# Kernel optimization log

Measured on AMD Instinct MI355X. Metric: run time of the kernel, lower is better.

## Reference

```python
import jax, jax.numpy as jnp
import numpy as np

N, E, G = 100000, 1600000, 1024
BN_EPS = 1e-5
NEG_SLOPE = 0.2


def setup_inputs() -> dict:
    key = jax.random.key(0)
    ks = jax.random.split(key, 8)
    x = jax.random.normal(ks[0], (N, 128), dtype=jnp.float32)
    edge_index = jax.random.randint(ks[1], (2, E), 0, N, dtype=jnp.int64)
    batch = jnp.sort(jax.random.randint(ks[2], (N,), 0, G, dtype=jnp.int64))
    Wl = jax.random.normal(ks[3], (3, 128, 128), dtype=jnp.float32) * 0.08
    bl = jnp.zeros((3, 128), dtype=jnp.float32)
    Wr = jax.random.normal(ks[4], (3, 128, 128), dtype=jnp.float32) * 0.08
    bn_gamma = jnp.ones((3, 128), dtype=jnp.float32)
    bn_beta = jnp.zeros((3, 128), dtype=jnp.float32)
    bn2_gamma = jnp.ones((128,), dtype=jnp.float32)
    bn2_beta = jnp.zeros((128,), dtype=jnp.float32)
    fc_W = jax.random.normal(ks[5], (128, 64), dtype=jnp.float32) * 0.08
    fc_b = jnp.zeros((64,), dtype=jnp.float32)
    return {"x": x, "edge_index": edge_index, "batch": batch, "Wl": Wl, "bl": bl,
            "Wr": Wr, "bn_gamma": bn_gamma, "bn_beta": bn_beta,
            "bn2_gamma": bn2_gamma, "bn2_beta": bn2_beta, "fc_W": fc_W, "fc_b": fc_b}


def _batch_norm(h, gamma, beta):
    # training-mode BatchNorm1d: batch statistics, biased variance
    mu = jnp.mean(h, axis=0)
    var = jnp.mean((h - mu) ** 2, axis=0)
    return gamma * (h - mu) * jax.lax.rsqrt(var + BN_EPS) + beta


def reference(x, edge_index, batch, Wl, bl, Wr, bn_gamma, bn_beta,
              bn2_gamma, bn2_beta, fc_W, fc_b):
    src, dst = edge_index[0], edge_index[1]
    # in-degree of each destination node (for mean aggregation)
    deg = jax.ops.segment_sum(jnp.ones((E,), dtype=x.dtype), dst, num_segments=N)
    inv_deg = jnp.where(deg > 0, 1.0 / jnp.maximum(deg, 1.0), 0.0)[:, None]  # [N,1]
    h = x
    for i in range(3):
        # SAGEConv: out = lin_l(mean_{j in N(i)} h_j) + lin_r(h_i)
        agg = jax.ops.segment_sum(h[src], dst, num_segments=N) * inv_deg  # [N,H]
        h = agg @ Wl[i] + bl[i] + h @ Wr[i]
        h = jax.nn.leaky_relu(_batch_norm(h, bn_gamma[i], bn_beta[i]), NEG_SLOPE)
        # dropout omitted (eval-mode / deterministic reference)
    pooled = jax.ops.segment_sum(h, batch, num_segments=G)  # [G,H] global_add_pool
    out = _batch_norm(pooled, bn2_gamma, bn2_beta) @ fc_W + fc_b  # [G,latent]
    return out
```

## Files before the change

kernel.cpp:

```cpp
#include <hip/hip_runtime.h>

#define HD 128
#define NCOPY 32
#define BSH 8
#define BSZ 256
#define EPB 4096

typedef __attribute__((ext_vector_type(8))) short short8;
typedef __attribute__((ext_vector_type(4))) float f32x4;

union ABu { unsigned long long u[2]; short8 s8; };

__device__ inline float bf2f(ushort u) {
    union { unsigned int i; float f; } x; x.i = ((unsigned int)u) << 16; return x.f;
}
__device__ inline float bflo(unsigned int u) {
    union { unsigned int i; float f; } x; x.i = u << 16; return x.f;
}
__device__ inline float bfhi(unsigned int u) {
    union { unsigned int i; float f; } x; x.i = u & 0xffff0000u; return x.f;
}
__device__ inline ushort f2bf(float f) {
    union { float f; unsigned int i; } x; x.f = f;
    unsigned int r = x.i + 0x7FFF + ((x.i >> 16) & 1);
    return (ushort)(r >> 16);
}


__global__ __launch_bounds__(256) void kp_count(const int* __restrict__ dst,
                                                int* __restrict__ bucketCount, int E, int NB) {
    __shared__ int hist[512];
    for (int i = threadIdx.x; i < NB; i += 256) hist[i] = 0;
    __syncthreads();
    int e0 = blockIdx.x * EPB;
#pragma unroll
    for (int j = 0; j < 16; ++j) {
        int e = e0 + j * 256 + threadIdx.x;
        if (e < E) atomicAdd(&hist[dst[e] >> BSH], 1);
    }
    __syncthreads();
    for (int i = threadIdx.x; i < NB; i += 256)
        if (hist[i]) atomicAdd(&bucketCount[i], hist[i]);
}

__global__ void kp_scan(const int* __restrict__ bucketCount, int* __restrict__ bucketBase,
                        int* __restrict__ gCursor, int NB, int E) {
    __shared__ int lds[512];
    int tid = threadIdx.x;
    int v = (tid < NB) ? bucketCount[tid] : 0;
    lds[tid] = v;
    __syncthreads();
    for (int off = 1; off < 512; off <<= 1) {
        int t = 0;
        if (tid >= off) t = lds[tid - off];
        __syncthreads();
        if (tid >= off) lds[tid] += t;
        __syncthreads();
    }
    int excl = lds[tid] - v;
    if (tid < NB) { bucketBase[tid] = excl; gCursor[tid] = excl; }
    if (tid == 0) bucketBase[NB] = E;
}

__global__ __launch_bounds__(256) void kp_part(const int* __restrict__ src,
                                               const int* __restrict__ dst,
                                               int* __restrict__ gCursor,
                                               unsigned int* __restrict__ packed, int E, int NB) {
    __shared__ int hist[512], lbase[512], lcur[512];
    for (int i = threadIdx.x; i < NB; i += 256) hist[i] = 0;
    __syncthreads();
    int e0 = blockIdx.x * EPB;
    int b[16]; unsigned int w[16];
#pragma unroll
    for (int j = 0; j < 16; ++j) {
        int e = e0 + j * 256 + threadIdx.x;
        b[j] = -1;
        if (e < E) {
            int d = dst[e];
            int s = src[e];
            b[j] = d >> BSH;
            w[j] = (unsigned int)s | (((unsigned int)d & (BSZ - 1)) << 17);
            atomicAdd(&hist[b[j]], 1);
        }
    }
    __syncthreads();
    for (int i = threadIdx.x; i < NB; i += 256) {
        int c = hist[i];
        lbase[i] = c ? atomicAdd(&gCursor[i], c) : 0;
        lcur[i] = 0;
    }
    __syncthreads();
#pragma unroll
    for (int j = 0; j < 16; ++j) {
        if (b[j] >= 0) {
            int r = atomicAdd(&lcur[b[j]], 1);
            packed[lbase[b[j]] + r] = w[j];
        }
    }
}

__global__ __launch_bounds__(256) void kp_degscan(const unsigned int* __restrict__ packed,
                                                  const int* __restrict__ bucketBase,
                                                  int* __restrict__ rowptr,
                                                  float* __restrict__ inv, int N, int E) {
    __shared__ int dcnt[BSZ];
    __shared__ int scn[BSZ];
    int bkt = blockIdx.x;
    int tid = threadIdx.x;
    int n0 = bkt << BSH;
    dcnt[tid] = 0;
    __syncthreads();
    int beg = bucketBase[bkt], end = bucketBase[bkt + 1];
    for (int e = beg + tid; e < end; e += 256)
        atomicAdd(&dcnt[packed[e] >> 17], 1);
    __syncthreads();
    int v = dcnt[tid];
    scn[tid] = v;
    __syncthreads();
    for (int off = 1; off < 256; off <<= 1) {
        int t = 0;
        if (tid >= off) t = scn[tid - off];
        __syncthreads();
        if (tid >= off) scn[tid] += t;
        __syncthreads();
    }
    int n = n0 + tid;
    if (n < N) {
        rowptr[n] = beg + scn[tid] - v;
        inv[n] = (v > 0) ? (1.0f / (float)v) : 0.0f;
    }
    if (bkt == 0 && tid == 0) rowptr[N] = E;
}

__global__ __launch_bounds__(256) void kp_fill(const unsigned int* __restrict__ packed,
                                               const int* __restrict__ bucketBase,
                                               const int* __restrict__ rowptr,
                                               int* __restrict__ csr, int N) {
    __shared__ int rp[BSZ];
    __shared__ int cur[BSZ];
    int bkt = blockIdx.x;
    int n0 = bkt << BSH;
    for (int i = threadIdx.x; i < BSZ; i += 256) {
        int n = n0 + i;
        rp[i] = (n < N) ? rowptr[n] : 0;
        cur[i] = 0;
    }
    __syncthreads();
    int beg = bucketBase[bkt], end = bucketBase[bkt + 1];
    for (int e = beg + threadIdx.x; e < end; e += 256) {
        unsigned int wv = packed[e];
        int ld = wv >> 17;
        int s = (int)(wv & 0x1FFFF);
        int p = atomicAdd(&cur[ld], 1);
        csr[rp[ld] + p] = s;
    }
}

__global__ void k_cvt(const float* __restrict__ in, ushort* __restrict__ out, int total4) {
    int i = blockIdx.x * blockDim.x + threadIdx.x;
    int stride = gridDim.x * blockDim.x;
    for (int idx = i; idx < total4; idx += stride) {
        float4 v = ((const float4*)in)[idx];
        ushort4 o;
        o.x = f2bf(v.x); o.y = f2bf(v.y); o.z = f2bf(v.z); o.w = f2bf(v.w);
        ((ushort4*)out)[idx] = o;
    }
}

__global__ void k_wt(const float* __restrict__ Wl, const float* __restrict__ Wr,
                     ushort* __restrict__ WT, int total) {
    int i = blockIdx.x * blockDim.x + threadIdx.x;
    if (i >= total) return;
    int l = i >> 15;
    int rem = i & 32767;
    int col = rem >> 8;
    int k = rem & 255;
    float v = (k < 128) ? Wl[l * 16384 + k * 128 + col] : Wr[l * 16384 + (k - 128) * 128 + col];
    WT[i] = f2bf(v);
}

__global__ __launch_bounds__(256) void k_agg(const ushort* __restrict__ h,
                                             const int* __restrict__ rowptr,
                                             const int* __restrict__ csr,
                                             const float* __restrict__ inv,
                                             ushort* __restrict__ agg, int N) {
    int node = blockIdx.x * 4 + (threadIdx.x >> 6);
    if (node >= N) return;
    int lane = threadIdx.x & 63;
    int g = lane >> 4, ln = lane & 15;
    int beg = rowptr[node], end = rowptr[node + 1];
    float a[8], b[8], c[8], d[8];
#pragma unroll
    for (int j = 0; j < 8; ++j) { a[j] = 0.f; b[j] = 0.f; c[j] = 0.f; d[j] = 0.f; }
    for (int e = beg + g; e < end; e += 16) {
        int s0 = csr[e];
        uint4 v0 = *(const uint4*)&h[(size_t)s0 * HD + ln * 8];
        int e1 = e + 4, e2 = e + 8, e3 = e + 12;
        if (e1 < end) {
            int s1 = csr[e1];
            uint4 v1 = *(const uint4*)&h[(size_t)s1 * HD + ln * 8];
            b[0] += bflo(v1.x); b[1] += bfhi(v1.x);
            b[2] += bflo(v1.y); b[3] += bfhi(v1.y);
            b[4] += bflo(v1.z); b[5] += bfhi(v1.z);
            b[6] += bflo(v1.w); b[7] += bfhi(v1.w);
        }
        if (e2 < end) {
            int s2 = csr[e2];
            uint4 v2 = *(const uint4*)&h[(size_t)s2 * HD + ln * 8];
            c[0] += bflo(v2.x); c[1] += bfhi(v2.x);
            c[2] += bflo(v2.y); c[3] += bfhi(v2.y);
            c[4] += bflo(v2.z); c[5] += bfhi(v2.z);
            c[6] += bflo(v2.w); c[7] += bfhi(v2.w);
        }
        if (e3 < end) {
            int s3 = csr[e3];
            uint4 v3 = *(const uint4*)&h[(size_t)s3 * HD + ln * 8];
            d[0] += bflo(v3.x); d[1] += bfhi(v3.x);
            d[2] += bflo(v3.y); d[3] += bfhi(v3.y);
            d[4] += bflo(v3.z); d[5] += bfhi(v3.z);
            d[6] += bflo(v3.w); d[7] += bfhi(v3.w);
        }
        a[0] += bflo(v0.x); a[1] += bfhi(v0.x);
        a[2] += bflo(v0.y); a[3] += bfhi(v0.y);
        a[4] += bflo(v0.z); a[5] += bfhi(v0.z);
        a[6] += bflo(v0.w); a[7] += bfhi(v0.w);
    }
#pragma unroll
    for (int j = 0; j < 8; ++j) {
        a[j] += b[j] + (c[j] + d[j]);
        a[j] += __shfl_xor(a[j], 16);
        a[j] += __shfl_xor(a[j], 32);
    }
    if (lane < 16) {
        float iv = inv[node];
        ushort o[8];
#pragma unroll
        for (int j = 0; j < 8; ++j) o[j] = f2bf(a[j] * iv);
        *(uint4*)&agg[(size_t)node * HD + ln * 8] = *(uint4*)o;
    }
}

__global__ __launch_bounds__(256) void k_gemm(
        const ushort* __restrict__ X1, const ushort* __restrict__ X2,
        const ushort* __restrict__ WT, const float* __restrict__ bias,
        ushort* __restrict__ out, float* __restrict__ stats, int N) {
    __shared__ ushort As[128 * 40];
    __shared__ ushort Bs[128 * 40];
    int tid = threadIdx.x;
    int lane = tid & 63, wid = tid >> 6;
    int wr = wid >> 1, wc = wid & 1;
    int ln15 = lane & 15, kg = lane >> 4;
    int rbase = blockIdx.x * 128;

    f32x4 acc[4][4];
#pragma unroll
    for (int m = 0; m < 4; ++m)
#pragma unroll
        for (int nn = 0; nn < 4; ++nn) acc[m][nn] = (f32x4){0.f, 0.f, 0.f, 0.f};

    for (int c = 0; c < 8; ++c) {
        const ushort* X = (c < 4) ? X1 : X2;
        int cb = (c & 3) * 32;
#pragma unroll
        for (int p = 0; p < 2; ++p) {
            int g = tid + p * 256;
            int r = g >> 2, q = g & 3;
            int grow = rbase + r;
            uint4 v = {0u, 0u, 0u, 0u};
            if (grow < N) v = *(const uint4*)&X[(size_t)grow * HD + cb + q * 8];
            *(uint4*)&As[r * 40 + q * 8] = v;
        }
#pragma unroll
        for (int p = 0; p < 2; ++p) {
            int g = tid + p * 256;
            int col = g >> 2, q = g & 3;
            *(uint4*)&Bs[col * 40 + q * 8] = *(const uint4*)&WT[col * 256 + c * 32 + q * 8];
        }
        __syncthreads();
        short8 af[4], bfr[4];
#pragma unroll
        for (int m = 0; m < 4; ++m) {
            int row = wr * 64 + m * 16 + ln15;
            const ushort* pa = &As[row * 40 + kg * 4];
            ABu u; u.u[0] = *(const unsigned long long*)pa;
            u.u[1] = *(const unsigned long long*)(pa + 16);
            af[m] = u.s8;
        }
#pragma unroll
        for (int nn = 0; nn < 4; ++nn) {
            int col = wc * 64 + nn * 16 + ln15;
            const ushort* pb = &Bs[col * 40 + kg * 4];
            ABu u; u.u[0] = *(const unsigned long long*)pb;
            u.u[1] = *(const unsigned long long*)(pb + 16);
            bfr[nn] = u.s8;
        }
#pragma unroll
        for (int m = 0; m < 4; ++m)
#pragma unroll
            for (int nn = 0; nn < 4; ++nn)
                acc[m][nn] = __builtin_amdgcn_mfma_f32_16x16x32_bf16(af[m], bfr[nn], acc[m][nn], 0, 0, 0);
        __syncthreads();
    }

    float s[4] = {0.f, 0.f, 0.f, 0.f};
    float q[4] = {0.f, 0.f, 0.f, 0.f};
    float bv[4];
#pragma unroll
    for (int nn = 0; nn < 4; ++nn) bv[nn] = bias[wc * 64 + nn * 16 + ln15];
#pragma unroll
    for (int m = 0; m < 4; ++m) {
#pragma unroll
        for (int j = 0; j < 4; ++j) {
            int row = rbase + wr * 64 + m * 16 + kg * 4 + j;
            if (row < N) {
#pragma unroll
                for (int nn = 0; nn < 4; ++nn) {
                    float v = acc[m][nn][j] + bv[nn];
                    out[(size_t)row * HD + wc * 64 + nn * 16 + ln15] = f2bf(v);
                    s[nn] += v; q[nn] += v * v;
                }
            }
        }
    }
#pragma unroll
    for (int nn = 0; nn < 4; ++nn) {
        s[nn] += __shfl_xor(s[nn], 16); s[nn] += __shfl_xor(s[nn], 32);
        q[nn] += __shfl_xor(q[nn], 16); q[nn] += __shfl_xor(q[nn], 32);
    }
    if (lane < 16) {
        int slot = (blockIdx.x & (NCOPY - 1)) * 256;
#pragma unroll
        for (int nn = 0; nn < 4; ++nn) {
            int col = wc * 64 + nn * 16 + lane;
            atomicAdd(&stats[slot + col], s[nn]);
            atomicAdd(&stats[slot + 128 + col], q[nn]);
        }
    }
}

__global__ void k_bnfin(const float* __restrict__ stats, const float* __restrict__ gamma,
                        const float* __restrict__ beta, float* __restrict__ bnp, float count) {
    int c = threadIdx.x;
    float s = 0.f, q = 0.f;
    for (int i = 0; i < NCOPY; ++i) { s += stats[i * 256 + c]; q += stats[i * 256 + 128 + c]; }
    float mean = s / count;
    float var = q / count - mean * mean;
    var = fmaxf(var, 0.f);
    float scale = gamma[c] * rsqrtf(var + 1e-5f);
    bnp[c] = scale;
    bnp[128 + c] = beta[c] - mean * scale;
}

__global__ void k_apply(ushort* buf, const float* __restrict__ bnp, int total8) {
    int i = blockIdx.x * blockDim.x + threadIdx.x;
    int stride = gridDim.x * blockDim.x;
    for (int idx = i; idx < total8; idx += stride) {
        int cb = (idx * 8) & (HD - 1);
        uint4 v = ((const uint4*)buf)[idx];
        float f[8];
        f[0] = bflo(v.x); f[1] = bfhi(v.x);
        f[2] = bflo(v.y); f[3] = bfhi(v.y);
        f[4] = bflo(v.z); f[5] = bfhi(v.z);
        f[6] = bflo(v.w); f[7] = bfhi(v.w);
        ushort o[8];
#pragma unroll
        for (int j = 0; j < 8; ++j) {
            float y = f[j] * bnp[cb + j] + bnp[128 + cb + j];
            y = (y > 0.f) ? y : 0.2f * y;
            o[j] = f2bf(y);
        }
        ((uint4*)buf)[idx] = *(uint4*)o;
    }
}

__global__ void k_poolapply(const ushort* __restrict__ h, const float* __restrict__ bnp,
                            const int* __restrict__ batch, float* __restrict__ pooled, int N) {
    int c = threadIdx.x;
    float sc = bnp[c], sh = bnp[128 + c];
    int n0 = blockIdx.x * 16;
    if (n0 >= N) return;
    int nend = min(n0 + 16, N);
    float acc = 0.f;
    int cur = batch[n0];
    for (int n = n0; n < nend; ++n) {
        int b = batch[n];
        if (b != cur) { atomicAdd(&pooled[cur * HD + c], acc); acc = 0.f; cur = b; }
        float y = bf2f(h[(size_t)n * HD + c]) * sc + sh;
        y = (y > 0.f) ? y : 0.2f * y;
        acc += y;
    }
    atomicAdd(&pooled[cur * HD + c], acc);
}

__global__ void k_colstats(const float* __restrict__ X, float* __restrict__ stats, int rows) {
    int c = threadIdx.x;
    float s = 0.f, q = 0.f;
    for (int r = blockIdx.x; r < rows; r += gridDim.x) {
        float v = X[r * HD + c];
        s += v; q += v * v;
    }
    int slot = (blockIdx.x & (NCOPY - 1)) * 256;
    atomicAdd(&stats[slot + c], s);
    atomicAdd(&stats[slot + 128 + c], q);
}

__global__ void k_final(const float* __restrict__ pooled, const float* __restrict__ bnp,
                        const float* __restrict__ fcW, const float* __restrict__ fcb,
                        float* __restrict__ outp, int G) {
    __shared__ float Wlds[HD * 64];
    __shared__ float prow[HD];
    int tid = threadIdx.x;
    for (int i = tid; i < HD * 64 / 4; i += 64) ((float4*)Wlds)[i] = ((const float4*)fcW)[i];
    int g = blockIdx.x;
    for (int c = tid; c < HD; c += 64) prow[c] = pooled[g * HD + c] * bnp[c] + bnp[128 + c];
    __syncthreads();
    float acc = fcb[tid];
#pragma unroll 8
    for (int c = 0; c < HD; ++c) acc += prow[c] * Wlds[c * 64 + tid];
    outp[g * 64 + tid] = acc;
}

extern "C" void kernel_launch(void* const* d_in, const int* in_sizes, int n_in,
                              void* d_out, int out_size, void* d_ws, size_t ws_size,
                              hipStream_t stream) {
    const float* x     = (const float*)d_in[0];
    const int*   ei    = (const int*)d_in[1];
    const int*   batch = (const int*)d_in[2];
    const float* Wl    = (const float*)d_in[3];
    const float* bl    = (const float*)d_in[4];
    const float* Wr    = (const float*)d_in[5];
    const float* bng   = (const float*)d_in[6];
    const float* bnb   = (const float*)d_in[7];
    const float* bn2g  = (const float*)d_in[8];
    const float* bn2b  = (const float*)d_in[9];
    const float* fcW   = (const float*)d_in[10];
    const float* fcb   = (const float*)d_in[11];

    int N = in_sizes[0] / HD;
    int E = in_sizes[1] / 2;
    int G = out_size / 64;
    const int* src = ei;
    const int* dst = ei + E;

    char* p = (char*)d_ws;
    auto alloc = [&](size_t bytes) -> void* {
        void* r = (void*)p;
        p += (bytes + 255) & ~(size_t)255;
        return r;
    };
    int NB = (N + BSZ - 1) >> BSH;
    int nPB = (E + EPB - 1) / EPB;

    int*    rowptr   = (int*)alloc((size_t)(N + 1) * 4);
    int*    bCount   = (int*)alloc((size_t)NB * 4);
    int*    bBase    = (int*)alloc((size_t)(NB + 1) * 4);
    int*    gCursor  = (int*)alloc((size_t)NB * 4);
    int*    csr      = (int*)alloc((size_t)E * 4);
    float*  inv      = (float*)alloc((size_t)N * 4);
    ushort* WT       = (ushort*)alloc((size_t)3 * 128 * 256 * 2);
    ushort* xb       = (ushort*)alloc((size_t)N * HD * 2);
    ushort* aggb     = (ushort*)alloc((size_t)N * HD * 2);
    ushort* hb1      = (ushort*)alloc((size_t)N * HD * 2);
    ushort* hb2      = (ushort*)alloc((size_t)N * HD * 2);
    float*  statsAll = (float*)alloc((size_t)3 * NCOPY * 256 * 4);
    float*  stats2   = (float*)alloc((size_t)NCOPY * 256 * 4);
    float*  bnp      = (float*)alloc(256 * 4);
    float*  pooled   = (float*)alloc((size_t)G * HD * 4);

    float* stats0 = statsAll;
    float* stats1 = statsAll + NCOPY * 256;
    float* statsL2 = statsAll + 2 * NCOPY * 256;

    unsigned int* packed = (unsigned int*)aggb;

    float* outp = (float*)d_out;
    int total4 = N * HD / 4;
    int total8 = N * HD / 8;
    int ggrid = (N + 127) / 128;
    int agrid = (N + 3) / 4;

    hipMemsetAsync(statsAll, 0, (size_t)3 * NCOPY * 256 * 4, stream);
    hipMemsetAsync(stats2, 0, (size_t)NCOPY * 256 * 4, stream);
    hipMemsetAsync(pooled, 0, (size_t)G * HD * 4, stream);
    hipMemsetAsync(bCount, 0, (size_t)NB * 4, stream);
    k_cvt<<<2048, 256, 0, stream>>>(x, xb, total4);
    k_wt<<<(3 * 128 * 256 + 255) / 256, 256, 0, stream>>>(Wl, Wr, WT, 3 * 128 * 256);

    kp_count<<<nPB, 256, 0, stream>>>(dst, bCount, E, NB);
    kp_scan<<<1, 512, 0, stream>>>(bCount, bBase, gCursor, NB, E);
    kp_part<<<nPB, 256, 0, stream>>>(src, dst, gCursor, packed, E, NB);
    kp_degscan<<<NB, 256, 0, stream>>>(packed, bBase, rowptr, inv, N, E);
    kp_fill<<<NB, 256, 0, stream>>>(packed, bBase, rowptr, csr, N);

    k_agg<<<agrid, 256, 0, stream>>>(xb, rowptr, csr, inv, aggb, N);
    k_gemm<<<ggrid, 256, 0, stream>>>(aggb, xb, WT, bl, hb1, stats0, N);
    k_bnfin<<<1, 128, 0, stream>>>(stats0, bng, bnb, bnp, (float)N);
    k_apply<<<2048, 256, 0, stream>>>(hb1, bnp, total8);

    k_agg<<<agrid, 256, 0, stream>>>(hb1, rowptr, csr, inv, aggb, N);
    k_gemm<<<ggrid, 256, 0, stream>>>(aggb, hb1, WT + 32768, bl + 128, hb2, stats1, N);
    k_bnfin<<<1, 128, 0, stream>>>(stats1, bng + 128, bnb + 128, bnp, (float)N);
    k_apply<<<2048, 256, 0, stream>>>(hb2, bnp, total8);

    k_agg<<<agrid, 256, 0, stream>>>(hb2, rowptr, csr, inv, aggb, N);
    k_gemm<<<ggrid, 256, 0, stream>>>(aggb, hb2, WT + 65536, bl + 256, hb1, statsL2, N);
    k_bnfin<<<1, 128, 0, stream>>>(statsL2, bng + 256, bnb + 256, bnp, (float)N);
    k_poolapply<<<(N + 15) / 16, HD, 0, stream>>>(hb1, bnp, batch, pooled, N);

    k_colstats<<<64, HD, 0, stream>>>(pooled, stats2, G);
    k_bnfin<<<1, 128, 0, stream>>>(stats2, bn2g, bn2b, bnp, (float)G);
    k_final<<<G, 64, 0, stream>>>(pooled, bnp, fcW, fcb, outp, G);
}
```

Baseline: 420.8 us.

## Fuse degree scan with CSR fill, shrink agg unroll, widen GEMM K-tile

Merges the degree-scan and CSR-fill kernels into one, so each bucket's packed edges are read by a single kernel that keeps the row pointers in shared memory, saving a launch and a rowptr reload. Cuts the aggregation loop's unroll from four to two independent gathers per iteration, which lowers register pressure but also reduces memory-level parallelism. Doubles the GEMM K-chunk to 64, halving the number of load/sync rounds at the cost of more LDS per block.

Result: faster. 411.4 us (-2.2%).

```diff
diff --git a/kernel.cpp b/kernel.cpp
--- a/kernel.cpp
+++ b/kernel.cpp
@@ -99,12 +99,14 @@
     }
 }
 
-__global__ __launch_bounds__(256) void kp_degscan(const unsigned int* __restrict__ packed,
+__global__ __launch_bounds__(256) void kp_degfill(const unsigned int* __restrict__ packed,
                                                   const int* __restrict__ bucketBase,
                                                   int* __restrict__ rowptr,
-                                                  float* __restrict__ inv, int N, int E) {
+                                                  float* __restrict__ inv,
+                                                  int* __restrict__ csr, int N, int E) {
     __shared__ int dcnt[BSZ];
     __shared__ int scn[BSZ];
+    __shared__ int rp[BSZ];
     int bkt = blockIdx.x;
     int tid = threadIdx.x;
     int n0 = bkt << BSH;
@@ -124,35 +126,22 @@
         if (tid >= off) scn[tid] += t;
         __syncthreads();
     }
+    int rpv = beg + scn[tid] - v;
     int n = n0 + tid;
     if (n < N) {
-        rowptr[n] = beg + scn[tid] - v;
+        rowptr[n] = rpv;
         inv[n] = (v > 0) ? (1.0f / (float)v) : 0.0f;
     }
     if (bkt == 0 && tid == 0) rowptr[N] = E;
-}
-
-__global__ __launch_bounds__(256) void kp_fill(const unsigned int* __restrict__ packed,
-                                               const int* __restrict__ bucketBase,
-                                               const int* __restrict__ rowptr,
-                                               int* __restrict__ csr, int N) {
-    __shared__ int rp[BSZ];
-    __shared__ int cur[BSZ];
-    int bkt = blockIdx.x;
-    int n0 = bkt << BSH;
-    for (int i = threadIdx.x; i < BSZ; i += 256) {
-        int n = n0 + i;
-        rp[i] = (n < N) ? rowptr[n] : 0;
-        cur[i] = 0;
-    }
-    __syncthreads();
-    int beg = bucketBase[bkt], end = bucketBase[bkt + 1];
-    for (int e = beg + threadIdx.x; e < end; e += 256) {
+    __syncthreads();
+    dcnt[tid] = 0;
+    rp[tid] = rpv;
+    __syncthreads();
+    for (int e = beg + tid; e < end; e += 256) {
         unsigned int wv = packed[e];
         int ld = wv >> 17;
-        int s = (int)(wv & 0x1FFFF);
-        int p = atomicAdd(&cur[ld], 1);
-        csr[rp[ld] + p] = s;
+        int p = atomicAdd(&dcnt[ld], 1);
+        csr[rp[ld] + p] = (int)(wv & 0x1FFFF);
     }
 }
 
@@ -189,13 +178,13 @@
     int lane = threadIdx.x & 63;
     int g = lane >> 4, ln = lane & 15;
     int beg = rowptr[node], end = rowptr[node + 1];
-    float a[8], b[8], c[8], d[8];
-#pragma unroll
-    for (int j = 0; j < 8; ++j) { a[j] = 0.f; b[j] = 0.f; c[j] = 0.f; d[j] = 0.f; }
-    for (int e = beg + g; e < end; e += 16) {
+    float a[8], b[8];
+#pragma unroll
+    for (int j = 0; j < 8; ++j) { a[j] = 0.f; b[j] = 0.f; }
+    for (int e = beg + g; e < end; e += 8) {
         int s0 = csr[e];
         uint4 v0 = *(const uint4*)&h[(size_t)s0 * HD + ln * 8];
-        int e1 = e + 4, e2 = e + 8, e3 = e + 12;
+        int e1 = e + 4;
         if (e1 < end) {
             int s1 = csr[e1];
             uint4 v1 = *(const uint4*)&h[(size_t)s1 * HD + ln * 8];
@@ -204,22 +193,6 @@
             b[4] += bflo(v1.z); b[5] += bfhi(v1.z);
             b[6] += bflo(v1.w); b[7] += bfhi(v1.w);
         }
-        if (e2 < end) {
-            int s2 = csr[e2];
-            uint4 v2 = *(const uint4*)&h[(size_t)s2 * HD + ln * 8];
-            c[0] += bflo(v2.x); c[1] += bfhi(v2.x);
-            c[2] += bflo(v2.y); c[3] += bfhi(v2.y);
-            c[4] += bflo(v2.z); c[5] += bfhi(v2.z);
-            c[6] += bflo(v2.w); c[7] += bfhi(v2.w);
-        }
-        if (e3 < end) {
-            int s3 = csr[e3];
-            uint4 v3 = *(const uint4*)&h[(size_t)s3 * HD + ln * 8];
-            d[0] += bflo(v3.x); d[1] += bfhi(v3.x);
-            d[2] += bflo(v3.y); d[3] += bfhi(v3.y);
-            d[4] += bflo(v3.z); d[5] += bfhi(v3.z);
-            d[6] += bflo(v3.w); d[7] += bfhi(v3.w);
-        }
         a[0] += bflo(v0.x); a[1] += bfhi(v0.x);
         a[2] += bflo(v0.y); a[3] += bfhi(v0.y);
         a[4] += bflo(v0.z); a[5] += bfhi(v0.z);
@@ -227,7 +200,7 @@
     }
 #pragma unroll
     for (int j = 0; j < 8; ++j) {
-        a[j] += b[j] + (c[j] + d[j]);
+        a[j] += b[j];
         a[j] += __shfl_xor(a[j], 16);
         a[j] += __shfl_xor(a[j], 32);
     }
@@ -244,8 +217,8 @@
         const ushort* __restrict__ X1, const ushort* __restrict__ X2,
         const ushort* __restrict__ WT, const float* __restrict__ bias,
         ushort* __restrict__ out, float* __restrict__ stats, int N) {
-    __shared__ ushort As[128 * 40];
-    __shared__ ushort Bs[128 * 40];
+    __shared__ ushort As[128 * 72];
+    __shared__ ushort Bs[128 * 72];
     int tid = threadIdx.x;
     int lane = tid & 63, wid = tid >> 6;
     int wr = wid >> 1, wc = wid & 1;
@@ -258,47 +231,50 @@
 #pragma unroll
         for (int nn = 0; nn < 4; ++nn) acc[m][nn] = (f32x4){0.f, 0.f, 0.f, 0.f};
 
-    for (int c = 0; c < 8; ++c) {
-        const ushort* X = (c < 4) ? X1 : X2;
-        int cb = (c & 3) * 32;
-#pragma unroll
-        for (int p = 0; p < 2; ++p) {
+    for (int c = 0; c < 4; ++c) {
+        const ushort* X = (c < 2) ? X1 : X2;
+        int cb = (c & 1) * 64;
+#pragma unroll
+        for (int p = 0; p < 4; ++p) {
             int g = tid + p * 256;
-            int r = g >> 2, q = g & 3;
+            int r = g >> 3, q = g & 7;
             int grow = rbase + r;
             uint4 v = {0u, 0u, 0u, 0u};
             if (grow < N) v = *(const uint4*)&X[(size_t)grow * HD + cb + q * 8];
-            *(uint4*)&As[r * 40 + q * 8] = v;
-        }
-#pragma unroll
-        for (int p = 0; p < 2; ++p) {
+            *(uint4*)&As[r * 72 + q * 8] = v;
+        }
+#pragma unroll
+        for (int p = 0; p < 4; ++p) {
             int g = tid + p * 256;
-            int col = g >> 2, q = g & 3;
-            *(uint4*)&Bs[col * 40 + q * 8] = *(const uint4*)&WT[col * 256 + c * 32 + q * 8];
-        }
-        __syncthreads();
-        short8 af[4], bfr[4];
-#pragma unroll
-        for (int m = 0; m < 4; ++m) {
-            int row = wr * 64 + m * 16 + ln15;
-            const ushort* pa = &As[row * 40 + kg * 4];
-            ABu u; u.u[0] = *(const unsigned long long*)pa;
-            u.u[1] = *(const unsigned long long*)(pa + 16);
-            af[m] = u.s8;
-        }
-#pragma unroll
-        for (int nn = 0; nn < 4; ++nn) {
-            int col = wc * 64 + nn * 16 + ln15;
-            const ushort* pb = &Bs[col * 40 + kg * 4];
-            ABu u; u.u[0] = *(const unsigned long long*)pb;
-            u.u[1] = *(const unsigned long long*)(pb + 16);
-            bfr[nn] = u.s8;
-        }
-#pragma unroll
-        for (int m = 0; m < 4; ++m)
-#pragma unroll
-            for (int nn = 0; nn < 4; ++nn)
-                acc[m][nn] = __builtin_amdgcn_mfma_f32_16x16x32_bf16(af[m], bfr[nn], acc[m][nn], 0, 0, 0);
+            int col = g >> 3, q = g & 7;
+            *(uint4*)&Bs[col * 72 + q * 8] = *(const uint4*)&WT[col * 256 + c * 64 + q * 8];
+        }
+        __syncthreads();
+#pragma unroll
+        for (int kk = 0; kk < 2; ++kk) {
+            short8 af[4], bfr[4];
+#pragma unroll
+            for (int m = 0; m < 4; ++m) {
+                int row = wr * 64 + m * 16 + ln15;
+                const ushort* pa = &As[row * 72 + kk * 32 + kg * 4];
+                ABu u; u.u[0] = *(const unsigned long long*)pa;
+                u.u[1] = *(const unsigned long long*)(pa + 16);
+                af[m] = u.s8;
+            }
+#pragma unroll
+            for (int nn = 0; nn < 4; ++nn) {
+                int col = wc * 64 + nn * 16 + ln15;
+                const ushort* pb = &Bs[col * 72 + kk * 32 + kg * 4];
+                ABu u; u.u[0] = *(const unsigned long long*)pb;
+                u.u[1] = *(const unsigned long long*)(pb + 16);
+                bfr[nn] = u.s8;
+            }
+#pragma unroll
+            for (int m = 0; m < 4; ++m)
+#pragma unroll
+                for (int nn = 0; nn < 4; ++nn)
+                    acc[m][nn] = __builtin_amdgcn_mfma_f32_16x16x32_bf16(af[m], bfr[nn], acc[m][nn], 0, 0, 0);
+        }
         __syncthreads();
     }
 
@@ -489,8 +465,7 @@
     kp_count<<<nPB, 256, 0, stream>>>(dst, bCount, E, NB);
     kp_scan<<<1, 512, 0, stream>>>(bCount, bBase, gCursor, NB, E);
     kp_part<<<nPB, 256, 0, stream>>>(src, dst, gCursor, packed, E, NB);
-    kp_degscan<<<NB, 256, 0, stream>>>(packed, bBase, rowptr, inv, N, E);
-    kp_fill<<<NB, 256, 0, stream>>>(packed, bBase, rowptr, csr, N);
+    kp_degfill<<<NB, 256, 0, stream>>>(packed, bBase, rowptr, inv, csr, N, E);
 
     k_agg<<<agrid, 256, 0, stream>>>(xb, rowptr, csr, inv, aggb, N);
     k_gemm<<<ggrid, 256, 0, stream>>>(aggb, xb, WT, bl, hb1, stats0, N);
```
